# Performance work log

Hardware: AMD Instinct MI355X
Metric: run time of the kernel (lower is better)

## Reference

```python
import jax, jax.numpy as jnp
import numpy as np


def sign_ste(x):
    # forward: sign(x); backward: grad * (|x| <= 1)  (straight-through estimator)
    # clip has exactly the STE gradient mask; stop_gradient swaps in sign(x) for fwd value.
    c = jnp.clip(x, -1.0, 1.0)
    return c + jax.lax.stop_gradient(jnp.sign(x) - c)


def setup_inputs() -> dict:
    key = jax.random.key(0)
    k1, k2, k3 = jax.random.split(key, 3)
    N, CIN, COUT = 8192, 4096, 4096
    input_x = jax.random.normal(k1, (N, CIN), dtype=jnp.float32)
    weight = jax.random.normal(k2, (COUT, CIN), dtype=jnp.float32) * 0.02
    bias = jax.random.normal(k3, (COUT,), dtype=jnp.float32) * 0.01
    return {"input_x": input_x, "weight": weight, "bias": bias}


def reference(input_x, weight, bias):
    qw = sign_ste(weight)            # [COUT, CIN], values in {-1, 0, +1}
    qx = sign_ste(input_x)           # [N, CIN]
    out = jnp.einsum('nc,oc->no', qx, qw)  # binary GEMM executed as float matmul
    alpha = jnp.mean(jnp.abs(weight))
    betta = jnp.mean(jnp.abs(input_x))
    return out * alpha * betta + bias
```

## Files before the change

### kernel.cpp

```cpp
#include <hip/hip_runtime.h>
#include <stdint.h>

#define N_ROWS 8192
#define C_IN   4096
#define C_OUT  4096
#define NCHUNK (C_IN / 64)
#define MT4    65536

typedef int   v4i  __attribute__((ext_vector_type(4)));
typedef int   v8i  __attribute__((ext_vector_type(8)));
typedef float v16f __attribute__((ext_vector_type(16)));

__global__ void pack_all_kernel(const float* __restrict__ x,
                                const float* __restrict__ w,
                                uint8_t* __restrict__ xf,
                                uint8_t* __restrict__ wf,
                                float* __restrict__ partials) {
    __shared__ __align__(16) uint16_t tile16[4096];
    __shared__ float sacc[4];

    const int b = blockIdx.x;
    const float* src; uint8_t* dst; int slab;
    if (b < 2048) { src = x; dst = xf; slab = b; }
    else          { src = w; dst = wf; slab = b - 2048; }
    const int mt = slab >> 3, cg = slab & 7;

    const int t = threadIdx.x;
    const int r = t >> 3, lc = t & 7;

    const float4* base = (const float4*)(src + (size_t)(mt * 32 + r) * C_IN + cg * 512) + lc;
    float acc = 0.f;
#pragma unroll
    for (int it = 0; it < 16; ++it) {
        float4 v = base[it * 8];
        uint16_t nv = (uint16_t)((v.x > 0.f ? 0x2u : 0xAu)
                               | (v.y > 0.f ? 0x2u : 0xAu) << 4
                               | (v.z > 0.f ? 0x2u : 0xAu) << 8
                               | (v.w > 0.f ? 0x2u : 0xAu) << 12);
        acc += fabsf(v.x) + fabsf(v.y) + fabsf(v.z) + fabsf(v.w);
        tile16[it * 256 + t] = nv;
    }
    __syncthreads();
    uint4* gout = (uint4*)(dst + (size_t)mt * MT4 + (size_t)cg * 8192);
    const uint4* lin = (const uint4*)tile16;
#pragma unroll
    for (int p = 0; p < 2; ++p) gout[p * 256 + t] = lin[p * 256 + t];

    for (int off = 32; off > 0; off >>= 1) acc += __shfl_down(acc, off, 64);
    const int lane = t & 63, wv = t >> 6;
    if (lane == 0) sacc[wv] = acc;
    __syncthreads();
    if (t == 0) {
        float s = 0.f;
        for (int i = 0; i < 4; ++i) s += sacc[i];
        partials[b] = s;
    }
}

__global__ void finalize_kernel(const float* __restrict__ part_x, int nx,
                                const float* __restrict__ part_w, int nw,
                                float* __restrict__ out_ab) {
    __shared__ float s[256];
    float ax = 0.f;
    for (int i = threadIdx.x; i < nx; i += 256) ax += part_x[i];
    s[threadIdx.x] = ax; __syncthreads();
    for (int st = 128; st > 0; st >>= 1) {
        if (threadIdx.x < st) s[threadIdx.x] += s[threadIdx.x + st];
        __syncthreads();
    }
    float sumx = s[0];
    __syncthreads();
    float aw = 0.f;
    for (int i = threadIdx.x; i < nw; i += 256) aw += part_w[i];
    s[threadIdx.x] = aw; __syncthreads();
    for (int st = 128; st > 0; st >>= 1) {
        if (threadIdx.x < st) s[threadIdx.x] += s[threadIdx.x + st];
        __syncthreads();
    }
    if (threadIdx.x == 0) {
        float sumw = s[0];
        float alpha = sumw / (float)((long long)C_OUT * C_IN);
        float betta = sumx / (float)((long long)N_ROWS * C_IN);
        out_ab[0] = alpha * betta;
    }
}

#define MFMA_FP4(a, b, c) \
    __builtin_amdgcn_mfma_scale_f32_32x32x64_f8f6f4((a), (b), (c), 4, 4, 0, 127, 0, 127)

__launch_bounds__(512)
__global__ void xnor_gemm_fp4(const uint8_t* __restrict__ Afrag,
                              const uint8_t* __restrict__ Bfrag,
                              const float* __restrict__ bias,
                              const float* __restrict__ ab_ptr,
                              float* __restrict__ out) {
    __shared__ __align__(16) uint8_t lds[4][2][8192];

    const int t    = threadIdx.x;
    const int lane = t & 63;
    const int hi   = lane >> 5;
    const int r    = lane & 31;
    const int wid  = t >> 6;
    const int wr   = wid >> 2;
    const int wc   = wid & 3;

    const int id  = blockIdx.x;
    const int swz = (id & 7) * 64 + (id >> 3);
    const int brow = (swz >> 4) * 256;
    const int bcol = (swz & 15) * 256;

    const uint8_t* Abase = Afrag + (size_t)(brow >> 5) * MT4;
    const uint8_t* Bbase = Bfrag + (size_t)(bcol >> 5) * MT4;
    const size_t soff = (size_t)(t >> 6) * MT4 + (size_t)(t & 63) * 16;

#define STG(buf, c)                                                                     \
    do {                                                                                \
        __builtin_amdgcn_global_load_lds(                                               \
            (const __attribute__((address_space(1))) void*)(Abase + soff + (size_t)(c) * 1024), \
            (__attribute__((address_space(3))) void*)(&lds[buf][0][t * 16]), 16, 0, 0); \
        __builtin_amdgcn_global_load_lds(                                               \
            (const __attribute__((address_space(1))) void*)(Bbase + soff + (size_t)(c) * 1024), \
            (__attribute__((address_space(3))) void*)(&lds[buf][1][t * 16]), 16, 0, 0); \
    } while (0)

    v16f acc[4][2] = {};

    STG(0, 0); STG(1, 1);

#pragma unroll 4
    for (int ck = 0; ck < NCHUNK; ++ck) {
        const int buf = ck & 3;
        if (ck < NCHUNK - 2) { asm volatile("s_waitcnt vmcnt(2)" ::: "memory"); }
        else                 { asm volatile("s_waitcnt vmcnt(0)" ::: "memory"); }
        __builtin_amdgcn_s_barrier();

        v4i a4[4], b4[2];
#pragma unroll
        for (int m = 0; m < 4; ++m)
            a4[m] = *(const v4i*)(&lds[buf][0][((wr * 4 + m) * 64 + lane) * 16]);
#pragma unroll
        for (int n = 0; n < 2; ++n)
            b4[n] = *(const v4i*)(&lds[buf][1][((wc * 2 + n) * 64 + lane) * 16]);

        if (ck + 2 < NCHUNK) STG((ck + 2) & 3, ck + 2);

        v8i a8[4], b8[2];
#pragma unroll
        for (int m = 0; m < 4; ++m) {
            v8i v = {a4[m][0], a4[m][1], a4[m][2], a4[m][3], 0, 0, 0, 0};
            a8[m] = v;
        }
#pragma unroll
        for (int n = 0; n < 2; ++n) {
            v8i v = {b4[n][0], b4[n][1], b4[n][2], b4[n][3], 0, 0, 0, 0};
            b8[n] = v;
        }

        __builtin_amdgcn_s_setprio(1);
#pragma unroll
        for (int m = 0; m < 4; ++m)
#pragma unroll
            for (int n = 0; n < 2; ++n)
                acc[m][n] = MFMA_FP4(a8[m], b8[n], acc[m][n]);
        __builtin_amdgcn_s_setprio(0);
    }

    const float ab = ab_ptr[0];
#pragma unroll
    for (int m = 0; m < 4; ++m) {
#pragma unroll
        for (int n = 0; n < 2; ++n) {
            int col = bcol + wc * 64 + n * 32 + r;
            float bv = bias[col];
#pragma unroll
            for (int reg = 0; reg < 16; ++reg) {
                int rowf = (reg & 3) + 8 * (reg >> 2) + 4 * hi;
                int grow = brow + wr * 128 + m * 32 + rowf;
                out[(size_t)grow * C_OUT + col] = acc[m][n][reg] * ab + bv;
            }
        }
    }
#undef STG
}

extern "C" void kernel_launch(void* const* d_in, const int* in_sizes, int n_in,
                              void* d_out, int out_size, void* d_ws, size_t ws_size,
                              hipStream_t stream) {
    const float* x    = (const float*)d_in[0];
    const float* w    = (const float*)d_in[1];
    const float* bias = (const float*)d_in[2];
    float* out = (float*)d_out;

    char* ws = (char*)d_ws;
    float* red      = (float*)ws;
    float* partials = red + 16;
    uint8_t* xs  = (uint8_t*)(ws + 16384);
    uint8_t* wsg = xs + (size_t)N_ROWS * C_IN / 2;

    pack_all_kernel<<<3072, 256, 0, stream>>>(x, w, xs, wsg, partials);
    finalize_kernel<<<1, 256, 0, stream>>>(partials, 2048, partials + 2048, 1024, red);

    dim3 grid((N_ROWS / 256) * (C_OUT / 256));
    xnor_gemm_fp4<<<grid, 512, 0, stream>>>(xs, wsg, bias, red, out);
}
```

Measured before the change: 131.2 us.

## Shrink GEMM block tile to 128x256 with 128-deep K chunks and triple buffering

The FP4 MFMA GEMM moves from 256x256 block tiles to 128x256, so the grid doubles to 1024 blocks and each wave holds a 2x2 accumulator set instead of 4x2. Each pipeline stage now stages two 64-wide K slices (half the number of barriers per K) in a 3-deep LDS ring instead of 4, and launch bounds request 4 waves per SIMD. The aim is more blocks and better occupancy, with fewer barriers per unit of K work. The cost is lower A/B reuse per block, which raises global and LDS traffic per MFMA.

```diff
diff --git a/kernel.cpp b/kernel.cpp
--- a/kernel.cpp
+++ b/kernel.cpp
@@ -4,7 +4,7 @@
 #define N_ROWS 8192
 #define C_IN   4096
 #define C_OUT  4096
-#define NCHUNK (C_IN / 64)
+#define NCHUNK (C_IN / 128)
 #define MT4    65536
 
 typedef int   v4i  __attribute__((ext_vector_type(4)));
@@ -87,14 +87,15 @@
 
 #define MFMA_FP4(a, b, c) \
     __builtin_amdgcn_mfma_scale_f32_32x32x64_f8f6f4((a), (b), (c), 4, 4, 0, 127, 0, 127)
-
-__launch_bounds__(512)
+#define UP8(v4) __builtin_shufflevector((v4), (v4), 0, 1, 2, 3, -1, -1, -1, -1)
+
+__launch_bounds__(512, 4)
 __global__ void xnor_gemm_fp4(const uint8_t* __restrict__ Afrag,
                               const uint8_t* __restrict__ Bfrag,
                               const float* __restrict__ bias,
                               const float* __restrict__ ab_ptr,
                               float* __restrict__ out) {
-    __shared__ __align__(16) uint8_t lds[4][2][8192];
+    __shared__ __align__(16) uint8_t lds[3][24576];
 
     const int t    = threadIdx.x;
     const int lane = t & 63;
@@ -105,82 +106,84 @@
     const int wc   = wid & 3;
 
     const int id  = blockIdx.x;
-    const int swz = (id & 7) * 64 + (id >> 3);
-    const int brow = (swz >> 4) * 256;
+    const int swz = (id & 7) * 128 + (id >> 3);
+    const int brow = (swz >> 4) * 128;
     const int bcol = (swz & 15) * 256;
 
     const uint8_t* Abase = Afrag + (size_t)(brow >> 5) * MT4;
     const uint8_t* Bbase = Bfrag + (size_t)(bcol >> 5) * MT4;
-    const size_t soff = (size_t)(t >> 6) * MT4 + (size_t)(t & 63) * 16;
+
+    const int pA = t;
+    const int pB0 = t, pB1 = t + 512;
+    const size_t offA  = (size_t)(pA  >> 7) * MT4 + (size_t)((pA  >> 6) & 1) * 1024 + (size_t)(pA  & 63) * 16;
+    const size_t offB0 = (size_t)(pB0 >> 7) * MT4 + (size_t)((pB0 >> 6) & 1) * 1024 + (size_t)(pB0 & 63) * 16;
+    const size_t offB1 = (size_t)(pB1 >> 7) * MT4 + (size_t)((pB1 >> 6) & 1) * 1024 + (size_t)(pB1 & 63) * 16;
 
 #define STG(buf, c)                                                                     \
     do {                                                                                \
+        size_t ka = (size_t)(c) * 2048;                                                 \
         __builtin_amdgcn_global_load_lds(                                               \
-            (const __attribute__((address_space(1))) void*)(Abase + soff + (size_t)(c) * 1024), \
-            (__attribute__((address_space(3))) void*)(&lds[buf][0][t * 16]), 16, 0, 0); \
+            (const __attribute__((address_space(1))) void*)(Abase + offA + ka),         \
+            (__attribute__((address_space(3))) void*)(&lds[buf][t * 16]), 16, 0, 0);    \
         __builtin_amdgcn_global_load_lds(                                               \
-            (const __attribute__((address_space(1))) void*)(Bbase + soff + (size_t)(c) * 1024), \
-            (__attribute__((address_space(3))) void*)(&lds[buf][1][t * 16]), 16, 0, 0); \
+            (const __attribute__((address_space(1))) void*)(Bbase + offB0 + ka),        \
+            (__attribute__((address_space(3))) void*)(&lds[buf][8192 + pB0 * 16]), 16, 0, 0); \
+        __builtin_amdgcn_global_load_lds(                                               \
+            (const __attribute__((address_space(1))) void*)(Bbase + offB1 + ka),        \
+            (__attribute__((address_space(3))) void*)(&lds[buf][8192 + pB1 * 16]), 16, 0, 0); \
     } while (0)
 
-    v16f acc[4][2] = {};
+#define LDA(buf, m, ks) (*(const v4i*)(&lds[buf][((wr * 2 + (m)) * 2048) + (ks) * 1024 + lane * 16]))
+#define LDB(buf, n, ks) (*(const v4i*)(&lds[buf][8192 + ((wc * 2 + (n)) * 2048) + (ks) * 1024 + lane * 16]))
+
+    v16f acc[2][2] = {};
 
     STG(0, 0); STG(1, 1);
 
-#pragma unroll 4
     for (int ck = 0; ck < NCHUNK; ++ck) {
-        const int buf = ck & 3;
-        if (ck < NCHUNK - 2) { asm volatile("s_waitcnt vmcnt(2)" ::: "memory"); }
+        const int buf = ck % 3;
+        if (ck < NCHUNK - 1) { asm volatile("s_waitcnt vmcnt(3)" ::: "memory"); }
         else                 { asm volatile("s_waitcnt vmcnt(0)" ::: "memory"); }
         __builtin_amdgcn_s_barrier();
 
-        v4i a4[4], b4[2];
-#pragma unroll
-        for (int m = 0; m < 4; ++m)
-            a4[m] = *(const v4i*)(&lds[buf][0][((wr * 4 + m) * 64 + lane) * 16]);
-#pragma unroll
-        for (int n = 0; n < 2; ++n)
-            b4[n] = *(const v4i*)(&lds[buf][1][((wc * 2 + n) * 64 + lane) * 16]);
-
-        if (ck + 2 < NCHUNK) STG((ck + 2) & 3, ck + 2);
-
-        v8i a8[4], b8[2];
-#pragma unroll
-        for (int m = 0; m < 4; ++m) {
-            v8i v = {a4[m][0], a4[m][1], a4[m][2], a4[m][3], 0, 0, 0, 0};
-            a8[m] = v;
-        }
+        v4i a0 = LDA(buf, 0, 0), a1 = LDA(buf, 1, 0);
+        v4i b0 = LDB(buf, 0, 0), b1 = LDB(buf, 1, 0);
+        if (ck + 2 < NCHUNK) STG((ck + 2) % 3, ck + 2);
+        __builtin_amdgcn_s_setprio(1);
+        acc[0][0] = MFMA_FP4(UP8(a0), UP8(b0), acc[0][0]);
+        acc[0][1] = MFMA_FP4(UP8(a0), UP8(b1), acc[0][1]);
+        acc[1][0] = MFMA_FP4(UP8(a1), UP8(b0), acc[1][0]);
+        acc[1][1] = MFMA_FP4(UP8(a1), UP8(b1), acc[1][1]);
+        __builtin_amdgcn_s_setprio(0);
+
+        a0 = LDA(buf, 0, 1); a1 = LDA(buf, 1, 1);
+        b0 = LDB(buf, 0, 1); b1 = LDB(buf, 1, 1);
+        __builtin_amdgcn_s_setprio(1);
+        acc[0][0] = MFMA_FP4(UP8(a0), UP8(b0), acc[0][0]);
+        acc[0][1] = MFMA_FP4(UP8(a0), UP8(b1), acc[0][1]);
+        acc[1][0] = MFMA_FP4(UP8(a1), UP8(b0), acc[1][0]);
+        acc[1][1] = MFMA_FP4(UP8(a1), UP8(b1), acc[1][1]);
+        __builtin_amdgcn_s_setprio(0);
+    }
+
+    const float ab = ab_ptr[0];
+#pragma unroll
+    for (int m = 0; m < 2; ++m) {
 #pragma unroll
         for (int n = 0; n < 2; ++n) {
-            v8i v = {b4[n][0], b4[n][1], b4[n][2], b4[n][3], 0, 0, 0, 0};
-            b8[n] = v;
-        }
-
-        __builtin_amdgcn_s_setprio(1);
-#pragma unroll
-        for (int m = 0; m < 4; ++m)
-#pragma unroll
-            for (int n = 0; n < 2; ++n)
-                acc[m][n] = MFMA_FP4(a8[m], b8[n], acc[m][n]);
-        __builtin_amdgcn_s_setprio(0);
-    }
-
-    const float ab = ab_ptr[0];
-#pragma unroll
-    for (int m = 0; m < 4; ++m) {
-#pragma unroll
-        for (int n = 0; n < 2; ++n) {
-            int col = bcol + wc * 64 + n * 32 + r;
+            int col = bcol + (wc * 2 + n) * 32 + r;
             float bv = bias[col];
 #pragma unroll
             for (int reg = 0; reg < 16; ++reg) {
                 int rowf = (reg & 3) + 8 * (reg >> 2) + 4 * hi;
-                int grow = brow + wr * 128 + m * 32 + rowf;
+                int grow = brow + (wr * 2 + m) * 32 + rowf;
                 out[(size_t)grow * C_OUT + col] = acc[m][n][reg] * ab + bv;
             }
         }
     }
 #undef STG
+#undef LDA
+#undef LDB
 }
 
 extern "C" void kernel_launch(void* const* d_in, const int* in_sizes, int n_in,
@@ -200,6 +203,6 @@
     pack_all_kernel<<<3072, 256, 0, stream>>>(x, w, xs, wsg, partials);
     finalize_kernel<<<1, 256, 0, stream>>>(partials, 2048, partials + 2048, 1024, red);
 
-    dim3 grid((N_ROWS / 256) * (C_OUT / 256));
+    dim3 grid((N_ROWS / 128) * (C_OUT / 256));
     xnor_gemm_fp4<<<grid, 512, 0, stream>>>(xs, wsg, bias, red, out);
 }
```

Measured after the change: 128.0 us. 1.03x faster.

## Deepen GEMM pipeline with register double-buffered fragments and three-ahead prefetch

Applied to the files above, without the earlier changes.

Restructures the FP4 MFMA main loop so LDS fragments for the next chunk are read into a second register set while the current chunk's MFMAs run. Global-to-LDS prefetch now runs three chunks ahead instead of two, with matching vmcnt waits. The fragment zero-padding is replaced by shufflevector with undefined upper lanes, and launch bounds request two blocks per CU. This is meant to hide LDS read latency and global load latency behind the matrix ops, at the cost of more registers and more complex wait and barrier logic.

```diff
diff --git a/kernel.cpp b/kernel.cpp
--- a/kernel.cpp
+++ b/kernel.cpp
@@ -85,10 +85,13 @@
     }
 }
 
-#define MFMA_FP4(a, b, c) \
-    __builtin_amdgcn_mfma_scale_f32_32x32x64_f8f6f4((a), (b), (c), 4, 4, 0, 127, 0, 127)
-
-__launch_bounds__(512)
+#define MF(a, b, c) \
+    __builtin_amdgcn_mfma_scale_f32_32x32x64_f8f6f4( \
+        __builtin_shufflevector((a), (a), 0, 1, 2, 3, -1, -1, -1, -1), \
+        __builtin_shufflevector((b), (b), 0, 1, 2, 3, -1, -1, -1, -1), \
+        (c), 4, 4, 0, 127, 0, 127)
+
+__launch_bounds__(512, 2)
 __global__ void xnor_gemm_fp4(const uint8_t* __restrict__ Afrag,
                               const uint8_t* __restrict__ Bfrag,
                               const float* __restrict__ bias,
@@ -113,56 +116,69 @@
     const uint8_t* Bbase = Bfrag + (size_t)(bcol >> 5) * MT4;
     const size_t soff = (size_t)(t >> 6) * MT4 + (size_t)(t & 63) * 16;
 
-#define STG(buf, c)                                                                     \
+#define STG(BUF, c)                                                                     \
     do {                                                                                \
+        size_t ka = (size_t)(c) * 1024;                                                 \
         __builtin_amdgcn_global_load_lds(                                               \
-            (const __attribute__((address_space(1))) void*)(Abase + soff + (size_t)(c) * 1024), \
-            (__attribute__((address_space(3))) void*)(&lds[buf][0][t * 16]), 16, 0, 0); \
+            (const __attribute__((address_space(1))) void*)(Abase + soff + ka),         \
+            (__attribute__((address_space(3))) void*)(&lds[BUF][0][t * 16]), 16, 0, 0); \
         __builtin_amdgcn_global_load_lds(                                               \
-            (const __attribute__((address_space(1))) void*)(Bbase + soff + (size_t)(c) * 1024), \
-            (__attribute__((address_space(3))) void*)(&lds[buf][1][t * 16]), 16, 0, 0); \
+            (const __attribute__((address_space(1))) void*)(Bbase + soff + ka),         \
+            (__attribute__((address_space(3))) void*)(&lds[BUF][1][t * 16]), 16, 0, 0); \
+    } while (0)
+
+#define LOADFRAGS(AS, BS, BUF)                                                       \
+    do {                                                                             \
+        AS[0] = *(const v4i*)(&lds[BUF][0][((wr * 4 + 0) * 64 + lane) * 16]);        \
+        AS[1] = *(const v4i*)(&lds[BUF][0][((wr * 4 + 1) * 64 + lane) * 16]);        \
+        AS[2] = *(const v4i*)(&lds[BUF][0][((wr * 4 + 2) * 64 + lane) * 16]);        \
+        AS[3] = *(const v4i*)(&lds[BUF][0][((wr * 4 + 3) * 64 + lane) * 16]);        \
+        BS[0] = *(const v4i*)(&lds[BUF][1][((wc * 2 + 0) * 64 + lane) * 16]);        \
+        BS[1] = *(const v4i*)(&lds[BUF][1][((wc * 2 + 1) * 64 + lane) * 16]);        \
+    } while (0)
+
+#define DOMFMA(AS, BS)                                \
+    do {                                              \
+        acc[0][0] = MF(AS[0], BS[0], acc[0][0]);      \
+        acc[0][1] = MF(AS[0], BS[1], acc[0][1]);      \
+        acc[1][0] = MF(AS[1], BS[0], acc[1][0]);      \
+        acc[1][1] = MF(AS[1], BS[1], acc[1][1]);      \
+        acc[2][0] = MF(AS[2], BS[0], acc[2][0]);      \
+        acc[2][1] = MF(AS[2], BS[1], acc[2][1]);      \
+        acc[3][0] = MF(AS[3], BS[0], acc[3][0]);      \
+        acc[3][1] = MF(AS[3], BS[1], acc[3][1]);      \
+    } while (0)
+
+#define BODY(cexp, SBUF, NBUF, CA, CB, NA, NB)                                      \
+    do {                                                                            \
+        const int c_ = (cexp);                                                      \
+        if (c_ + 3 < NCHUNK) STG(SBUF, c_ + 3);                                     \
+        if (c_ + 1 < NCHUNK) {                                                      \
+            if (c_ < NCHUNK - 3)       { asm volatile("s_waitcnt vmcnt(4)" ::: "memory"); } \
+            else if (c_ == NCHUNK - 3) { asm volatile("s_waitcnt vmcnt(2)" ::: "memory"); } \
+            else                       { asm volatile("s_waitcnt vmcnt(0)" ::: "memory"); } \
+        }                                                                           \
+        asm volatile("s_waitcnt lgkmcnt(0)" ::: "memory");                          \
+        __builtin_amdgcn_s_barrier();                                               \
+        if (c_ + 1 < NCHUNK) LOADFRAGS(NA, NB, NBUF);                               \
+        __builtin_amdgcn_s_setprio(1);                                              \
+        DOMFMA(CA, CB);                                                             \
+        __builtin_amdgcn_s_setprio(0);                                              \
     } while (0)
 
     v16f acc[4][2] = {};
-
-    STG(0, 0); STG(1, 1);
-
-#pragma unroll 4
-    for (int ck = 0; ck < NCHUNK; ++ck) {
-        const int buf = ck & 3;
-        if (ck < NCHUNK - 2) { asm volatile("s_waitcnt vmcnt(2)" ::: "memory"); }
-        else                 { asm volatile("s_waitcnt vmcnt(0)" ::: "memory"); }
-        __builtin_amdgcn_s_barrier();
-
-        v4i a4[4], b4[2];
-#pragma unroll
-        for (int m = 0; m < 4; ++m)
-            a4[m] = *(const v4i*)(&lds[buf][0][((wr * 4 + m) * 64 + lane) * 16]);
-#pragma unroll
-        for (int n = 0; n < 2; ++n)
-            b4[n] = *(const v4i*)(&lds[buf][1][((wc * 2 + n) * 64 + lane) * 16]);
-
-        if (ck + 2 < NCHUNK) STG((ck + 2) & 3, ck + 2);
-
-        v8i a8[4], b8[2];
-#pragma unroll
-        for (int m = 0; m < 4; ++m) {
-            v8i v = {a4[m][0], a4[m][1], a4[m][2], a4[m][3], 0, 0, 0, 0};
-            a8[m] = v;
-        }
-#pragma unroll
-        for (int n = 0; n < 2; ++n) {
-            v8i v = {b4[n][0], b4[n][1], b4[n][2], b4[n][3], 0, 0, 0, 0};
-            b8[n] = v;
-        }
-
-        __builtin_amdgcn_s_setprio(1);
-#pragma unroll
-        for (int m = 0; m < 4; ++m)
-#pragma unroll
-            for (int n = 0; n < 2; ++n)
-                acc[m][n] = MFMA_FP4(a8[m], b8[n], acc[m][n]);
-        __builtin_amdgcn_s_setprio(0);
+    v4i A0[4], B0[2], A1[4], B1[2];
+
+    STG(0, 0); STG(1, 1); STG(2, 2);
+    asm volatile("s_waitcnt vmcnt(4)" ::: "memory");
+    __builtin_amdgcn_s_barrier();
+    LOADFRAGS(A0, B0, 0);
+
+    for (int cb = 0; cb < NCHUNK; cb += 4) {
+        BODY(cb + 0, 3, 1, A0, B0, A1, B1);
+        BODY(cb + 1, 0, 2, A1, B1, A0, B0);
+        BODY(cb + 2, 1, 3, A0, B0, A1, B1);
+        BODY(cb + 3, 2, 0, A1, B1, A0, B0);
     }
 
     const float ab = ab_ptr[0];
@@ -181,6 +197,9 @@
         }
     }
 #undef STG
+#undef LOADFRAGS
+#undef DOMFMA
+#undef BODY
 }
 
 extern "C" void kernel_launch(void* const* d_in, const int* in_sizes, int n_in,
```

Measured after the change: 140.2 us. 1.07x slower.
